# Kernel optimization log

Hardware: AMD Instinct MI355X
Metric: run time of the kernel (lower is better)

Reference implementation:

```python
import jax, jax.numpy as jnp
import numpy as np

BLANK = 0          # tf.nn.ctc_loss default blank_index (StringLookup reserves 0 for OOV)
PAD = 127          # padding_value = char_to_num.vocabulary_size()
NEG = -1e30        # log-space 'zero' (avoid -inf to keep grads NaN-free)
B, T, C, L = 1024, 256, 128, 32


def setup_inputs() -> dict:
    key = jax.random.key(0)
    k1, k2 = jax.random.split(key)
    # labels in [1, PAD-1]; none equal PAD so label_length == L (full-length labels)
    y_true = jax.random.randint(k1, (B, L), 1, PAD).astype(jnp.int32)
    y_pred = jax.random.normal(k2, (B, T, C), dtype=jnp.float32)
    return {"y_true": y_true, "y_pred": y_pred}


def _ctc_loss(y_true, y_pred):
    """Faithful jax version of tf.nn.ctc_loss(labels, logits, label_len, T,
    logits_time_major=False, blank_index=0): standard log-space alpha DP."""
    Bn, Tn, Cn = y_pred.shape
    Ln = y_true.shape[1]
    S = 2 * Ln + 1  # extended label length (blanks interleaved)

    logp = jax.nn.log_softmax(y_pred, axis=-1)                    # [B,T,C]

    # extended label sequence: blank, l1, blank, l2, ..., blank   # [B,S]
    ext = jnp.full((Bn, S), BLANK, dtype=y_true.dtype)
    ext = ext.at[:, 1::2].set(y_true)

    # log-probs gathered at extended-label symbols                # [B,T,S]
    lp_ext = jnp.take_along_axis(
        logp, jnp.broadcast_to(ext[:, None, :], (Bn, Tn, S)), axis=2)

    # label_length = count of non-padding entries (mirrors count_nonzero)
    label_len = jnp.sum(y_true != PAD, axis=1)                    # [B]

    # skip transition s-2 -> s allowed iff ext[s] is a non-blank differing
    # from ext[s-2]
    skip_ok = jnp.concatenate(
        [jnp.zeros((Bn, 2), bool),
         (ext[:, 2:] != BLANK) & (ext[:, 2:] != ext[:, :-2])], axis=1)  # [B,S]

    neg1 = jnp.full((Bn, 1), NEG, logp.dtype)
    neg2 = jnp.full((Bn, 2), NEG, logp.dtype)

    alpha0 = jnp.full((Bn, S), NEG, logp.dtype)
    alpha0 = alpha0.at[:, 0].set(lp_ext[:, 0, 0]).at[:, 1].set(lp_ext[:, 0, 1])

    def step(alpha, lp_t):  # alpha,[B,S]  lp_t,[B,S]
        a1 = jnp.concatenate([neg1, alpha[:, :-1]], axis=1)
        a2 = jnp.concatenate([neg2, alpha[:, :-2]], axis=1)
        a2 = jnp.where(skip_ok, a2, NEG)
        new = lp_t + jnp.logaddexp(jnp.logaddexp(alpha, a1), a2)
        return new, None

    lp_seq = jnp.transpose(lp_ext, (1, 0, 2))                     # [T,B,S]
    alphaT, _ = jax.lax.scan(step, alpha0, lp_seq[1:])            # [B,S]

    # total log-likelihood ends at last blank (2*len) or last label (2*len-1)
    bi = jnp.arange(Bn)
    e1 = 2 * label_len
    e2 = 2 * label_len - 1
    loglik = jnp.logaddexp(alphaT[bi, e1], alphaT[bi, e2])        # [B]
    return -loglik


def reference(y_true, y_pred):
    # The original layer returns y_pred and registers the loss via add_loss;
    # the compute-dominant quantity is the per-example CTC loss, returned here.
    return _ctc_loss(y_true, y_pred)
```

## Files before the change

kernel.cpp:

```cpp
#include <hip/hip_runtime.h>
#include <cstdint>


#define CTC_BLANK 0
#define CTC_PAD   127
#define NEG       (-1e30f)
#define LOG2E     1.44269504088896340736f
#define LN2       0.69314718055994530942f

constexpr int Bn = 1024, Tn = 256, Cn = 128, Ln = 32;
constexpr int NSLOT = Ln + 1;
constexpr int CR  = 16;
constexpr int NCH = Tn / CR;
constexpr int CF  = CR * Cn;

__device__ __forceinline__ float fexp2(float x) { return __builtin_amdgcn_exp2f(x); }
__device__ __forceinline__ float flog2(float x) { return __builtin_amdgcn_logf(x); }

template <int CTRL>
__device__ __forceinline__ float dpp_add(float s) {
    int v = __builtin_amdgcn_update_dpp(0, __float_as_int(s), CTRL, 0xF, 0xF, true);
    return s + __int_as_float(v);
}
__device__ __forceinline__ float dpp_wave_shr1(float src, float old) {
    return __int_as_float(__builtin_amdgcn_update_dpp(
        __float_as_int(old), __float_as_int(src), 0x138, 0xF, 0xF, false));
}
__device__ __forceinline__ void gl_lds16(const float* g, float* l) {
    __builtin_amdgcn_global_load_lds(
        (const __attribute__((address_space(1))) uint32_t*)g,
        (__attribute__((address_space(3))) uint32_t*)l, 16, 0, 0);
}

__global__ __launch_bounds__(512, 8) void ctc_fused_kernel(
        const int*   __restrict__ y_true,
        const float* __restrict__ y_pred,
        float*       __restrict__ out)
{
    __shared__ __align__(16) float raw[2][CF];
    __shared__ _Float16 Gc[Tn * NSLOT];
    __shared__ int   labels[Ln];
    __shared__ __align__(16) int cmap[Cn];
    __shared__ int   used[Cn];
    __shared__ int   wcnt[8];
    __shared__ float partS[16];
    __shared__ float aEs[64], aOs[64];

    const int b    = blockIdx.x;
    const int tid  = threadIdx.x;
    const int lane = tid & 63;
    const int wave = tid >> 6;

    const float* gbase = y_pred + (size_t)b * Tn * Cn;

    auto stage = [&](int c, int buf) {
        gl_lds16(gbase + c * CF + tid * 4, &raw[buf][wave * 256]);
    };

    stage(0, 0);

    if (tid < Ln) labels[tid] = y_true[b * Ln + tid];
    if (tid < Cn) used[tid] = 0;
    __syncthreads();
    if (tid == 0) used[CTC_BLANK] = 1;
    if (tid < Ln) used[labels[tid]] = 1;
    __syncthreads();
    {
        bool f = (tid < Cn) && (used[tid] != 0);
        unsigned long long m = __ballot(f);
        if (lane == 0) wcnt[wave] = __popcll(m);
        __syncthreads();
        int base = 0;
        for (int w = 0; w < wave; ++w) base += wcnt[w];
        if (tid < Cn)
            cmap[tid] = f ? (base + __popcll(m & ((1ull << lane) - 1ull))) : -1;
        __syncthreads();
    }

    const int half = lane >> 5;
    const int l32  = lane & 31;
    const int4 cm  = ((const int4*)cmap)[l32];
    float acc = 0.f;

    const int  i      = lane;
    const bool validO = (i < Ln);
    const bool validE = (i <= Ln);
    const int  myLab   = validO ? labels[i] : -1;
    const int  prevLab = (i >= 1 && i < Ln) ? labels[i - 1] : -1;
    const int  slotO   = validO ? cmap[myLab] : 0;
    const bool skipO   = (i >= 1 && i < Ln) &&
                         (myLab != CTC_BLANK) && (myLab != prevLab);
    const int  len = __popcll(__ballot(validO && (myLab != CTC_PAD)));
    float aE = NEG, aO = NEG;

    auto dp_chunk = [&](int t0, int t1) {
        int t = t0;
        if (t == 0) {
            aE = (i == 0) ? (float)Gc[0]     : NEG;
            aO = (i == 0) ? (float)Gc[slotO] : NEG;
            t = 1;
        } else {
            aE = aEs[i];
            aO = aOs[i];
        }
        float pB[2], pO[2];
        const int ta = t, tb = (t + 1 < t1) ? t + 1 : t1 - 1;
        pB[0] = (float)Gc[ta * NSLOT]; pO[0] = (float)Gc[ta * NSLOT + slotO];
        pB[1] = (float)Gc[tb * NSLOT]; pO[1] = (float)Gc[tb * NSLOT + slotO];
        int k = 0;
        #pragma unroll 2
        for (; t < t1; ++t) {
            const float lpB = pB[k], lpO = pO[k];
            const int tp = (t + 2 < t1) ? t + 2 : t1 - 1;
            pB[k] = (float)Gc[tp * NSLOT];
            pO[k] = (float)Gc[tp * NSLOT + slotO];
            k ^= 1;

            const float aOup = dpp_wave_shr1(aO, NEG);
            const float m  = fmaxf(aE, aOup);
            const float e1 = fexp2(aE - m);
            const float e2 = fexp2(aOup - m);
            const float sE = e1 + e2;
            const float nE = lpB + m + flog2(sE);
            const float m3 = fmaxf(aO, m);
            const float nO = lpO + m3 +
                flog2(fexp2(aO - m3) + (skipO ? sE : e1) * fexp2(m - m3));
            aE = validE ? nE : NEG;
            aO = validO ? nO : NEG;
        }
        aEs[i] = aE;
        aOs[i] = aO;
    };

    for (int c = 0; c < NCH; ++c) {
        if (c + 1 < NCH) stage(c + 1, (c + 1) & 1);

        if (c > 0 && wave == ((c - 1 + b) & 7))
            dp_chunk((c - 1) * CR, c * CR);

        __builtin_amdgcn_sched_barrier(0);
        if (c + 1 < NCH) asm volatile("s_waitcnt vmcnt(1)" ::: "memory");
        else             asm volatile("s_waitcnt vmcnt(0)" ::: "memory");
        __builtin_amdgcn_sched_barrier(0);

        {
            const int rl = 2 * wave + half;
            const int r  = c * CR + rl;
            const float4 x = ((const float4*)&raw[c & 1][rl * Cn])[l32];
            const float e0 = x.x * LOG2E, e1 = x.y * LOG2E,
                        e2 = x.z * LOG2E, e3 = x.w * LOG2E;
            if (cm.x >= 0) Gc[r * NSLOT + cm.x] = (_Float16)e0;
            if (cm.y >= 0) Gc[r * NSLOT + cm.y] = (_Float16)e1;
            if (cm.z >= 0) Gc[r * NSLOT + cm.z] = (_Float16)e2;
            if (cm.w >= 0) Gc[r * NSLOT + cm.w] = (_Float16)e3;
            float s = fexp2(e0) + fexp2(e1) + fexp2(e2) + fexp2(e3);
            s = dpp_add<0x111>(s);
            s = dpp_add<0x112>(s);
            s = dpp_add<0x114>(s);
            s = dpp_add<0x118>(s);
            s = dpp_add<0x142>(s);
            acc += flog2(s);
        }
        if (c == NCH - 1 && l32 == 31) partS[wave * 2 + half] = acc;

        asm volatile("s_waitcnt lgkmcnt(0)" ::: "memory");
        __builtin_amdgcn_s_barrier();
    }

    if (wave == ((NCH - 1 + b) & 7)) {
        dp_chunk(Tn - CR, Tn);
        const float v1 = __shfl(aE, len, 64);
        const float v2 = __shfl(aO, len - 1, 64);
        if (i == 0) {
            float S = 0.f;
            #pragma unroll
            for (int j = 0; j < 16; ++j) S += partS[j];
            const float mm = fmaxf(v1, v2);
            const float L2 = mm + flog2(fexp2(v1 - mm) + fexp2(v2 - mm));
            out[b] = LN2 * (S - L2);
        }
    }
}

extern "C" void kernel_launch(void* const* d_in, const int* in_sizes, int n_in,
                              void* d_out, int out_size, void* d_ws, size_t ws_size,
                              hipStream_t stream) {
    const int*   y_true = (const int*)d_in[0];
    const float* y_pred = (const float*)d_in[1];
    float*       out    = (float*)d_out;
    ctc_fused_kernel<<<Bn, 512, 0, stream>>>(y_true, y_pred, out);
}
```

Before: 203.4 us.

## Halve block to four waves with eight-row chunks to raise per-CU occupancy

Result: faster. 198.7 us (-2.3%).

```diff
diff --git a/kernel.cpp b/kernel.cpp
--- a/kernel.cpp
+++ b/kernel.cpp
@@ -10,7 +10,7 @@
 
 constexpr int Bn = 1024, Tn = 256, Cn = 128, Ln = 32;
 constexpr int NSLOT = Ln + 1;
-constexpr int CR  = 16;
+constexpr int CR  = 8;
 constexpr int NCH = Tn / CR;
 constexpr int CF  = CR * Cn;
 
@@ -32,7 +32,7 @@
         (__attribute__((address_space(3))) uint32_t*)l, 16, 0, 0);
 }
 
-__global__ __launch_bounds__(512, 8) void ctc_fused_kernel(
+__global__ __launch_bounds__(256, 6) void ctc_fused_kernel(
         const int*   __restrict__ y_true,
         const float* __restrict__ y_pred,
         float*       __restrict__ out)
@@ -41,23 +41,27 @@
     __shared__ _Float16 Gc[Tn * NSLOT];
     __shared__ int   labels[Ln];
     __shared__ __align__(16) int cmap[Cn];
-    __shared__ int   used[Cn];
-    __shared__ int   wcnt[8];
+    __shared__ int   wcnt[4];
     __shared__ float partS[16];
     __shared__ float aEs[64], aOs[64];
+    int* const used = (int*)raw[1];
 
     const int b    = blockIdx.x;
     const int tid  = threadIdx.x;
     const int lane = tid & 63;
     const int wave = tid >> 6;
+    const int half = lane >> 5;
+    const int l32  = lane & 31;
+    const int rotb = (b + (b >> 8)) & 3;
 
     const float* gbase = y_pred + (size_t)b * Tn * Cn;
 
-    auto stage = [&](int c, int buf) {
-        gl_lds16(gbase + c * CF + tid * 4, &raw[buf][wave * 256]);
-    };
-
-    stage(0, 0);
+    auto stage = [&](int c) {
+        gl_lds16(gbase + (size_t)(c * CR + 2 * wave) * Cn + lane * 4,
+                 &raw[c & 1][wave * 256]);
+    };
+
+    stage(0);
 
     if (tid < Ln) labels[tid] = y_true[b * Ln + tid];
     if (tid < Cn) used[tid] = 0;
@@ -77,10 +81,9 @@
         __syncthreads();
     }
 
-    const int half = lane >> 5;
-    const int l32  = lane & 31;
-    const int4 cm  = ((const int4*)cmap)[l32];
-    float acc = 0.f;
+    const int4 cm = ((const int4*)cmap)[l32];
+    const int rl = 2 * wave + half;
+    float accE = 0.f, accO = 0.f;
 
     const int  i      = lane;
     const bool validO = (i < Ln);
@@ -132,42 +135,47 @@
         aOs[i] = aO;
     };
 
-    for (int c = 0; c < NCH; ++c) {
-        if (c + 1 < NCH) stage(c + 1, (c + 1) & 1);
-
-        if (c > 0 && wave == ((c - 1 + b) & 7))
+    auto process = [&](int c, float& acc) {
+        const int r = c * CR + rl;
+        const float4 x = ((const float4*)&raw[c & 1][wave * 256 + half * 128])[l32];
+        const float e0 = x.x * LOG2E, e1 = x.y * LOG2E,
+                    e2 = x.z * LOG2E, e3 = x.w * LOG2E;
+        if (cm.x >= 0) Gc[r * NSLOT + cm.x] = (_Float16)e0;
+        if (cm.y >= 0) Gc[r * NSLOT + cm.y] = (_Float16)e1;
+        if (cm.z >= 0) Gc[r * NSLOT + cm.z] = (_Float16)e2;
+        if (cm.w >= 0) Gc[r * NSLOT + cm.w] = (_Float16)e3;
+        float s = fexp2(e0) + fexp2(e1) + fexp2(e2) + fexp2(e3);
+        s = dpp_add<0x111>(s);
+        s = dpp_add<0x112>(s);
+        s = dpp_add<0x114>(s);
+        s = dpp_add<0x118>(s);
+        s = dpp_add<0x142>(s);
+        acc += flog2(s);
+    };
+
+    auto iter = [&](int c, float& acc) {
+        if (c + 1 < NCH) stage(c + 1);
+        if (c > 0 && wave == ((c - 1 + rotb) & 3))
             dp_chunk((c - 1) * CR, c * CR);
-
         __builtin_amdgcn_sched_barrier(0);
         if (c + 1 < NCH) asm volatile("s_waitcnt vmcnt(1)" ::: "memory");
         else             asm volatile("s_waitcnt vmcnt(0)" ::: "memory");
         __builtin_amdgcn_sched_barrier(0);
-
-        {
-            const int rl = 2 * wave + half;
-            const int r  = c * CR + rl;
-            const float4 x = ((const float4*)&raw[c & 1][rl * Cn])[l32];
-            const float e0 = x.x * LOG2E, e1 = x.y * LOG2E,
-                        e2 = x.z * LOG2E, e3 = x.w * LOG2E;
-            if (cm.x >= 0) Gc[r * NSLOT + cm.x] = (_Float16)e0;
-            if (cm.y >= 0) Gc[r * NSLOT + cm.y] = (_Float16)e1;
-            if (cm.z >= 0) Gc[r * NSLOT + cm.z] = (_Float16)e2;
-            if (cm.w >= 0) Gc[r * NSLOT + cm.w] = (_Float16)e3;
-            float s = fexp2(e0) + fexp2(e1) + fexp2(e2) + fexp2(e3);
-            s = dpp_add<0x111>(s);
-            s = dpp_add<0x112>(s);
-            s = dpp_add<0x114>(s);
-            s = dpp_add<0x118>(s);
-            s = dpp_add<0x142>(s);
-            acc += flog2(s);
-        }
-        if (c == NCH - 1 && l32 == 31) partS[wave * 2 + half] = acc;
-
+        process(c, acc);
+        if (c == NCH - 1 && l32 == 31) {
+            partS[rl]     = accE;
+            partS[rl + 8] = accO;
+        }
         asm volatile("s_waitcnt lgkmcnt(0)" ::: "memory");
         __builtin_amdgcn_s_barrier();
+    };
+
+    for (int cc = 0; cc < NCH / 2; ++cc) {
+        iter(2 * cc,     accE);
+        iter(2 * cc + 1, accO);
     }
 
-    if (wave == ((NCH - 1 + b) & 7)) {
+    if (wave == ((NCH - 1 + rotb) & 3)) {
         dp_chunk(Tn - CR, Tn);
         const float v1 = __shfl(aE, len, 64);
         const float v2 = __shfl(aO, len - 1, 64);
@@ -188,5 +196,5 @@
     const int*   y_true = (const int*)d_in[0];
     const float* y_pred = (const float*)d_in[1];
     float*       out    = (float*)d_out;
-    ctc_fused_kernel<<<Bn, 512, 0, stream>>>(y_true, y_pred, out);
-}
+    ctc_fused_kernel<<<Bn, 256, 0, stream>>>(y_true, y_pred, out);
+}
```
